# Optimization experiments

Hardware: AMD Instinct MI355X
Metric: run time of the kernel (lower is better)

Reference implementation:

```python
import jax, jax.numpy as jnp
import numpy as np

EPS = 1e-08
TARGET_MARGIN = 1e-3


def setup_inputs() -> dict:
    key = jax.random.key(0)
    k1, k2, k3 = jax.random.split(key, 3)
    B, L, N = 256, 512, 4
    preds = jax.random.normal(k1, (B, L, N), dtype=jnp.float32)
    targets = jax.random.uniform(k2, (B, L, N), dtype=jnp.float32)
    masks = jax.random.randint(k3, (B, L, N), 0, 2).astype(jnp.bool_)
    return {"preds": preds, "targets": targets, "masks": masks}


def _bce_with_logits(x, t):
    # numerically stable binary_cross_entropy_with_logits, reduction='none'
    return jnp.maximum(x, 0.0) - x * t + jax.nn.softplus(-jnp.abs(x))


def reference(preds, targets, masks):
    B, L, N = preds.shape
    # valid ordered pairs: col > row (strict upper triangle over batch)
    pair = jnp.arange(B)[None, :] > jnp.arange(B)[:, None]  # (B, B)

    # scan over the (small) feature axis N to keep peak memory at one
    # (B, B, L) pairwise tensor at a time, matching the chunked original.
    ps = jnp.transpose(preds, (2, 0, 1))    # (N, B, L)
    ts = jnp.transpose(targets, (2, 0, 1))  # (N, B, L)
    ms = jnp.transpose(masks, (2, 0, 1))    # (N, B, L)

    def step(acc, xs):
        p, t, m = xs  # each (B, L)
        x = p[:, None, :] - p[None, :, :]                       # (B, B, L) pred diff
        tg = ((t[:, None, :] - t[None, :, :]) > TARGET_MARGIN).astype(p.dtype)
        mf = jnp.logical_and(jnp.logical_and(m[:, None, :], m[None, :, :]),
                             pair[:, :, None])                  # (B, B, L)
        mfl = mf.astype(p.dtype)
        bce = _bce_with_logits(x, tg)
        loss_sum = jnp.sum(bce * mfl)
        mask_sum = jnp.sum(mfl)
        loss_n = jnp.where(mask_sum > 0, loss_sum / (mask_sum + EPS), 0.0)
        return acc + loss_n, None

    total, _ = jax.lax.scan(step, jnp.zeros((), preds.dtype), (ps, ts, ms))
    return total / N
```

## Files before the change

kernel.cpp:

```cpp
#include <hip/hip_runtime.h>

constexpr int B    = 256;
constexpr int NCOL = 2048;

#define MARGIN 1e-3f
#define LOG2E  1.4426950408889634f
#define LN2    0.6931471805599453

constexpr size_t OFF_SLAB   = 0;
constexpr size_t OFF_CPAIRS = 8192;

__global__ __launch_bounds__(256) void col_pair_kernel(
    const float* __restrict__ preds,
    const float* __restrict__ targets,
    const int*   __restrict__ masks,
    float* __restrict__ slab,
    float* __restrict__ cpairs)
{
    const int col  = blockIdx.x;
    const int t    = threadIdx.x;
    const int lane = t & 63;
    const int wave = t >> 6;

    const int   mv = masks[t * NCOL + col];
    const float uv = preds[t * NCOL + col] * LOG2E;
    const float tv = targets[t * NCOL + col];

    __shared__ float2 sc[256];
    __shared__ int    wcnt[4];
    __shared__ float  s4[4];

    const unsigned long long bal = __ballot(mv != 0);
    if (lane == 0) wcnt[wave] = __popcll(bal);
    __syncthreads();

    int basr = 0;
    #pragma unroll
    for (int w = 0; w < 4; ++w) basr += (w < wave) ? wcnt[w] : 0;
    const int c = wcnt[0] + wcnt[1] + wcnt[2] + wcnt[3];

    if (mv) {
        const int rank = basr + __popcll(bal & ((1ull << lane) - 1ull));
        sc[rank] = make_float2(uv, tv);
    }
    __syncthreads();

    const int K   = (c >= 1) ? ((c - 1) >> 1) : 0;
    const int dlo = (wave * K) / 4 + 1;
    const int dhi = ((wave + 1) * K) / 4;

    float lg = 0.f;

    #pragma unroll
    for (int q = 0; q < 4; ++q) {
        const int a = lane + 64 * q;
        if (a < c) {
            const float2 av = sc[a];
            float pp = 1.f;
            for (int d = dlo; d <= dhi; ++d) {
                int b = a + d;
                const bool wr = (b >= c);
                b = wr ? b - c : b;
                const float2 bv = sc[b];
                const float x  = av.x - bv.x;
                const float td = av.y - bv.y;
                const bool pos = wr ? (td < -MARGIN) : (td > MARGIN);
                const float xp = (pos != wr) ? -x : x;
                pp *= (__builtin_exp2f(xp) + 1.0f);
                if ((d & 7) == 7) { lg += __builtin_log2f(pp); pp = 1.f; }
            }
            lg += __builtin_log2f(pp);
        }
    }

    if (wave == 3 && c >= 2 && (c & 1) == 0) {
        const int hc = c >> 1;
        float pp = 1.f;
        #pragma unroll
        for (int q = 0; q < 2; ++q) {
            const int a = lane + 64 * q;
            if (a < hc) {
                const float2 av = sc[a];
                const float2 bv = sc[a + hc];
                const float x  = av.x - bv.x;
                const float td = av.y - bv.y;
                const float xp = (td > MARGIN) ? -x : x;
                pp *= (__builtin_exp2f(xp) + 1.0f);
            }
        }
        lg += __builtin_log2f(pp);
    }

    #pragma unroll
    for (int off = 32; off > 0; off >>= 1)
        lg += __shfl_down(lg, off, 64);
    if (lane == 0) s4[wave] = lg;
    __syncthreads();

    if (t == 0) {
        slab[col]   = s4[0] + s4[1] + s4[2] + s4[3];
        cpairs[col] = (float)((c * (c - 1)) / 2);
    }
}

__global__ __launch_bounds__(256) void finalize_kernel(
    const float* __restrict__ slab,
    const float* __restrict__ cpairs,
    float* __restrict__ out)
{
    const int t = threadIdx.x;
    double ls = 0.0, cs = 0.0;
    for (int q = t; q < NCOL; q += 256) {
        ls += (double)slab[q];
        cs += (double)cpairs[q];
    }

    __shared__ double sl[256], sp[256], res[4];
    sl[t] = ls; sp[t] = cs;
    __syncthreads();

    if (t < 4) {
        double lsn = 0.0, csn = 0.0;
        for (int g = t; g < 256; g += 4) { lsn += sl[g]; csn += sp[g]; }
        res[t] = (csn > 0.0) ? (LN2 * lsn / (csn + 1e-8)) : 0.0;
    }
    __syncthreads();

    if (t == 0)
        out[0] = (float)((res[0] + res[1] + res[2] + res[3]) * 0.25);
}

extern "C" void kernel_launch(void* const* d_in, const int* in_sizes, int n_in,
                              void* d_out, int out_size, void* d_ws, size_t ws_size,
                              hipStream_t stream)
{
    const float* preds   = (const float*)d_in[0];
    const float* targets = (const float*)d_in[1];
    const int*   masks   = (const int*)d_in[2];
    float* out = (float*)d_out;

    char* ws = (char*)d_ws;
    float* slab   = (float*)(ws + OFF_SLAB);
    float* cpairs = (float*)(ws + OFF_CPAIRS);

    col_pair_kernel<<<NCOL, 256, 0, stream>>>(preds, targets, masks, slab, cpairs);
    finalize_kernel<<<1, 256, 0, stream>>>(slab, cpairs, out);
}
```

Baseline: 41.24 us.

## Add transpose pre-pass so pair kernel reads columns contiguously

Result: slower. 43.35 us (+5.1%).

```diff
diff --git a/kernel.cpp b/kernel.cpp
--- a/kernel.cpp
+++ b/kernel.cpp
@@ -9,11 +9,62 @@
 
 constexpr size_t OFF_SLAB   = 0;
 constexpr size_t OFF_CPAIRS = 8192;
-
-__global__ __launch_bounds__(256) void col_pair_kernel(
+constexpr size_t OFF_UT     = 65536;
+constexpr size_t OFF_TT     = 65536 + 2097152;
+constexpr size_t OFF_MT     = 65536 + 4194304;
+
+__global__ __launch_bounds__(256) void transpose_kernel(
     const float* __restrict__ preds,
     const float* __restrict__ targets,
     const int*   __restrict__ masks,
+    float*         __restrict__ uT,
+    float*         __restrict__ tT,
+    unsigned char* __restrict__ mT)
+{
+    const int t        = threadIdx.x;
+    const int row_tile = blockIdx.x >> 6;
+    const int col_tile = blockIdx.x & 63;
+    const int base_row = row_tile * 64;
+    const int base_col = col_tile * 32;
+
+    __shared__ float tile[64][33];
+
+    const int rr = t >> 5;
+    const int rc = t & 31;
+    const int wc = t >> 6;
+    const int wr = t & 63;
+
+    #pragma unroll
+    for (int p = 0; p < 8; ++p)
+        tile[p * 8 + rr][rc] = preds[(base_row + p * 8 + rr) * NCOL + base_col + rc] * LOG2E;
+    __syncthreads();
+    #pragma unroll
+    for (int q = 0; q < 8; ++q)
+        uT[(base_col + q * 4 + wc) * 256 + base_row + wr] = tile[wr][q * 4 + wc];
+    __syncthreads();
+
+    #pragma unroll
+    for (int p = 0; p < 8; ++p)
+        tile[p * 8 + rr][rc] = targets[(base_row + p * 8 + rr) * NCOL + base_col + rc];
+    __syncthreads();
+    #pragma unroll
+    for (int q = 0; q < 8; ++q)
+        tT[(base_col + q * 4 + wc) * 256 + base_row + wr] = tile[wr][q * 4 + wc];
+    __syncthreads();
+
+    #pragma unroll
+    for (int p = 0; p < 8; ++p)
+        tile[p * 8 + rr][rc] = (float)(masks[(base_row + p * 8 + rr) * NCOL + base_col + rc] != 0);
+    __syncthreads();
+    #pragma unroll
+    for (int q = 0; q < 8; ++q)
+        mT[(base_col + q * 4 + wc) * 256 + base_row + wr] = (unsigned char)(tile[wr][q * 4 + wc] != 0.f);
+}
+
+__global__ __launch_bounds__(256) void col_pair_kernel(
+    const float* __restrict__ uT,
+    const float* __restrict__ tT,
+    const unsigned char* __restrict__ mT,
     float* __restrict__ slab,
     float* __restrict__ cpairs)
 {
@@ -22,9 +73,9 @@
     const int lane = t & 63;
     const int wave = t >> 6;
 
-    const int   mv = masks[t * NCOL + col];
-    const float uv = preds[t * NCOL + col] * LOG2E;
-    const float tv = targets[t * NCOL + col];
+    const float        uv = uT[col * 256 + t];
+    const float        tv = tT[col * 256 + t];
+    const unsigned char mv = mT[col * 256 + t];
 
     __shared__ float2 sc[256];
     __shared__ int    wcnt[4];
@@ -59,13 +110,13 @@
             float pp = 1.f;
             for (int d = dlo; d <= dhi; ++d) {
                 int b = a + d;
-                const bool wr = (b >= c);
-                b = wr ? b - c : b;
+                const bool wr2 = (b >= c);
+                b = wr2 ? b - c : b;
                 const float2 bv = sc[b];
                 const float x  = av.x - bv.x;
                 const float td = av.y - bv.y;
-                const bool pos = wr ? (td < -MARGIN) : (td > MARGIN);
-                const float xp = (pos != wr) ? -x : x;
+                const bool pos = wr2 ? (td < -MARGIN) : (td > MARGIN);
+                const float xp = (pos != wr2) ? -x : x;
                 pp *= (__builtin_exp2f(xp) + 1.0f);
                 if ((d & 7) == 7) { lg += __builtin_log2f(pp); pp = 1.f; }
             }
@@ -140,9 +191,13 @@
     float* out = (float*)d_out;
 
     char* ws = (char*)d_ws;
-    float* slab   = (float*)(ws + OFF_SLAB);
-    float* cpairs = (float*)(ws + OFF_CPAIRS);
-
-    col_pair_kernel<<<NCOL, 256, 0, stream>>>(preds, targets, masks, slab, cpairs);
+    float*         slab   = (float*)(ws + OFF_SLAB);
+    float*         cpairs = (float*)(ws + OFF_CPAIRS);
+    float*         uT     = (float*)(ws + OFF_UT);
+    float*         tT     = (float*)(ws + OFF_TT);
+    unsigned char* mT     = (unsigned char*)(ws + OFF_MT);
+
+    transpose_kernel<<<256, 256, 0, stream>>>(preds, targets, masks, uT, tT, mT);
+    col_pair_kernel<<<NCOL, 256, 0, stream>>>(uT, tT, mT, slab, cpairs);
     finalize_kernel<<<1, 256, 0, stream>>>(slab, cpairs, out);
 }
```
